# Optimization experiments

Hardware: AMD Instinct MI355X
Metric: run time of the kernel (lower is better)

The kernel has to match this reference:

```python
import jax, jax.numpy as jnp
import numpy as np

B, S = 16384, 6
IN_SIZE = 128
FIN, NFIN, BERT = 84, 11, 768
D = IN_SIZE + FIN + NFIN + BERT  # 991 = mlp_in_dim
NODE_V = 6 * 50000 + 1
FIN_V = 100001
OUT = 2


def setup_inputs() -> dict:
    key = jax.random.key(0)
    ks = jax.random.split(key, 20)
    inp = {}
    inp["node_seq"] = jax.random.randint(ks[0], (B, S), 0, 300000)
    inp["fin_seq"] = jax.random.randint(ks[1], (B, S), 0, 100000)
    inp["nfin_seq"] = jax.random.randint(ks[2], (B, S), 0, 100000)
    inp["mda_seq"] = jax.random.randint(ks[3], (B, S), 0, 100000)
    inp["seq_len"] = 1 + jax.random.randint(ks[4], (B,), 0, S)  # in [1, S]
    # embedding tables
    inp["node_table"] = jax.random.normal(ks[5], (NODE_V, IN_SIZE), jnp.float32) * 0.02
    inp["fin_table"] = jax.random.normal(ks[6], (FIN_V, FIN), jnp.float32) * 0.02
    inp["nfin_table"] = jax.random.normal(ks[7], (FIN_V, NFIN), jnp.float32) * 0.02
    inp["bert_table"] = jax.random.normal(ks[8], (FIN_V, BERT), jnp.float32) * 0.02
    # LayerNorm params
    inp["ln_g"] = jnp.ones((D,), jnp.float32)
    inp["ln_b"] = jnp.zeros((D,), jnp.float32)
    # GRU params (torch layout: [3D, D] for reset|update|new)
    s = 1.0 / np.sqrt(D)
    inp["W_ih"] = jax.random.uniform(ks[9], (3 * D, D), jnp.float32, -s, s)
    inp["W_hh"] = jax.random.uniform(ks[10], (3 * D, D), jnp.float32, -s, s)
    inp["b_ih"] = jax.random.uniform(ks[11], (3 * D,), jnp.float32, -s, s)
    inp["b_hh"] = jax.random.uniform(ks[12], (3 * D,), jnp.float32, -s, s)
    # BatchNorm1d affine params
    inp["bn_g"] = jnp.ones((D,), jnp.float32)
    inp["bn_b"] = jnp.zeros((D,), jnp.float32)
    # MLP: Linear(D, 2D) -> Linear(2D, OUT)
    inp["W1"] = jax.random.uniform(ks[13], (2 * D, D), jnp.float32, -s, s)
    inp["b1"] = jax.random.uniform(ks[14], (2 * D,), jnp.float32, -s, s)
    s2 = 1.0 / np.sqrt(2 * D)
    inp["W2"] = jax.random.uniform(ks[15], (OUT, 2 * D), jnp.float32, -s2, s2)
    inp["b2"] = jax.random.uniform(ks[16], (OUT,), jnp.float32, -s2, s2)
    return inp


def _forward(node_seq, fin_seq, nfin_seq, mda_seq, seq_len,
             node_table, fin_table, nfin_table, bert_table,
             ln_g, ln_b, W_ih, W_hh, b_ih, b_hh, bn_g, bn_b, W1, b1, W2, b2):
    # embedding lookups -> concat  [B, S, D]
    x = jnp.concatenate([
        node_table[node_seq],
        fin_table[fin_seq],
        nfin_table[nfin_seq],
        bert_table[mda_seq],
    ], axis=-1)
    # LayerNorm (eps=1e-5, torch default)
    mu = jnp.mean(x, axis=-1, keepdims=True)
    var = jnp.mean(jnp.square(x - mu), axis=-1, keepdims=True)
    x = (x - mu) * jax.lax.rsqrt(var + 1e-5) * ln_g + ln_b
    # GRU, batch_first; precompute input projections [S, B, 3D]
    xg = jnp.einsum('bsd,gd->sbg', x, W_ih) + b_ih
    h0 = jnp.zeros((x.shape[0], W_hh.shape[1]), x.dtype)
    d = W_hh.shape[1]

    def step(h, xg_t):
        gh = h @ W_hh.T + b_hh
        xr, xz, xn = xg_t[:, :d], xg_t[:, d:2 * d], xg_t[:, 2 * d:]
        hr, hz, hn = gh[:, :d], gh[:, d:2 * d], gh[:, 2 * d:]
        r = jax.nn.sigmoid(xr + hr)
        z = jax.nn.sigmoid(xz + hz)
        n = jnp.tanh(xn + r * hn)
        h = (1.0 - z) * n + z * h
        return h, h

    _, ys = jax.lax.scan(step, h0, xg)          # [S, B, D]
    ys = jnp.transpose(ys, (1, 0, 2))           # [B, S, D]
    # gather_indexes at seq_len - 1
    idx = (seq_len - 1)[:, None, None]
    out = jnp.take_along_axis(ys, idx, axis=1)[:, 0, :]  # [B, D]
    # BatchNorm1d with batch stats (training math), eps=1e-4
    bmu = jnp.mean(out, axis=0)
    bvar = jnp.mean(jnp.square(out - bmu), axis=0)
    out = (out - bmu) * jax.lax.rsqrt(bvar + 1e-4) * bn_g + bn_b
    # MLP: two linears, no activation
    h1 = out @ W1.T + b1
    logits = h1 @ W2.T + b2
    return logits


def reference(node_seq, fin_seq, nfin_seq, mda_seq, seq_len,
              node_table, fin_table, nfin_table, bert_table,
              ln_g, ln_b, W_ih, W_hh, b_ih, b_hh, bn_g, bn_b, W1, b1, W2, b2):
    return _forward(node_seq, fin_seq, nfin_seq, mda_seq, seq_len,
                    node_table, fin_table, nfin_table, bert_table,
                    ln_g, ln_b, W_ih, W_hh, b_ih, b_hh, bn_g, bn_b, W1, b1, W2, b2)
```

## Files before the change

kernel.cpp:

```cpp
#include <hip/hip_runtime.h>
#include <hip/hip_bf16.h>
#include <cstdint>
#include <cstddef>

#define D_   991
#define DP   992
#define GP   3072
#define B_   16384
#define S_   6

typedef __bf16 bf16;
typedef __attribute__((ext_vector_type(8))) __bf16 bf16x8;
typedef __attribute__((ext_vector_type(4))) float f32x4;

#define GLDS16(gp, lp) __builtin_amdgcn_global_load_lds(               \
    (const __attribute__((address_space(1))) void*)(gp),               \
    (__attribute__((address_space(3))) void*)(lp), 16, 0, 0)

__global__ __launch_bounds__(256, 2) void gemm_bt2(
    const bf16* __restrict__ A0, const bf16* __restrict__ W0,
    float* __restrict__ C0,
    const bf16* __restrict__ A1, const bf16* __restrict__ W1,
    float* __restrict__ C1)
{
  __shared__ __align__(16) bf16 As[128 * 32];
  __shared__ __align__(16) bf16 Bs[128 * 32];

  const bf16* A = blockIdx.z ? A1 : A0;
  const bf16* W = blockIdx.z ? W1 : W0;
  float*      C = blockIdx.z ? C1 : C0;

  const int tid  = threadIdx.x;
  const int lane = tid & 63;
  const int wave = tid >> 6;
  const int bm = blockIdx.y;
  const int bn = blockIdx.x;

  const int srow = tid >> 2;
  const int scol = (tid & 3) << 3;
  const bf16* aP = A + (size_t)(bm * 128 + srow) * DP + scol;
  const bf16* bP = W + (size_t)(bn * 128 + srow) * DP + scol;
  bf16* asW = &As[wave * 512];
  bf16* bsW = &Bs[wave * 512];

  const int wr = (wave >> 1) << 6;
  const int wc = (wave & 1) << 6;
  const int frow = lane & 15;
  const int fq   = lane >> 4;

  f32x4 acc[4][4];
#pragma unroll
  for (int i = 0; i < 4; i++)
#pragma unroll
    for (int j = 0; j < 4; j++) acc[i][j] = (f32x4){0.f, 0.f, 0.f, 0.f};

  for (int k0 = 0; k0 < DP; k0 += 32) {
    __syncthreads();
    GLDS16(aP + k0,                     asW);
    GLDS16(aP + (size_t)64 * DP + k0,   asW + 2048);
    GLDS16(bP + k0,                     bsW);
    GLDS16(bP + (size_t)64 * DP + k0,   bsW + 2048);
    __syncthreads();

    bf16x8 af[4], bfr[4];
#pragma unroll
    for (int mt = 0; mt < 4; mt++)
      af[mt] = *(const bf16x8*)&As[(wr + mt * 16 + frow) * 32 + fq * 8];
#pragma unroll
    for (int nt = 0; nt < 4; nt++)
      bfr[nt] = *(const bf16x8*)&Bs[(wc + nt * 16 + frow) * 32 + fq * 8];
#pragma unroll
    for (int mt = 0; mt < 4; mt++)
#pragma unroll
      for (int nt = 0; nt < 4; nt++)
        acc[mt][nt] = __builtin_amdgcn_mfma_f32_16x16x32_bf16(
            af[mt], bfr[nt], acc[mt][nt], 0, 0, 0);
  }

  const int rbase = bm * 128 + wr + fq * 4;
  const int cbase = bn * 128 + wc + frow;
#pragma unroll
  for (int mt = 0; mt < 4; mt++)
#pragma unroll
    for (int nt = 0; nt < 4; nt++) {
      float* cp = C + (size_t)(rbase + mt * 16) * GP + cbase + nt * 16;
#pragma unroll
      for (int i = 0; i < 4; i++) cp[(size_t)i * GP] = acc[mt][nt][i];
    }
}

__global__ __launch_bounds__(256) void pad_w(
    const float* __restrict__ Wih, const float* __restrict__ Whh,
    bf16* __restrict__ Wihp, bf16* __restrict__ Whhp)
{
  int idx = blockIdx.x * 256 + threadIdx.x;
  if (idx >= GP * DP) return;
  int c = idx % DP;
  int p = idx / DP;
  int sec = p >> 10;
  int j = p & 1023;
  bf16 vi = (bf16)0.0f, vh = (bf16)0.0f;
  if (j < D_ && c < D_) {
    size_t src = ((size_t)sec * D_ + j) * D_ + c;
    vi = (bf16)Wih[src];
    vh = (bf16)Whh[src];
  }
  Wihp[idx] = vi;
  Whhp[idx] = vh;
}

#define WCJ 16
__global__ __launch_bounds__(256) void wc_fold(
    const float* __restrict__ W1, const float* __restrict__ b1,
    const float* __restrict__ W2, const float* __restrict__ b2,
    float* __restrict__ wc)
{
  const int o   = blockIdx.y;
  const int j0  = blockIdx.x * WCJ;
  const int tid = threadIdx.x;
  const int jend = min(j0 + WCJ, 2 * D_);

  float acc[4] = {0.f, 0.f, 0.f, 0.f};
  for (int j = j0; j < jend; j++) {
    float w2 = W2[o * 2 * D_ + j];
#pragma unroll
    for (int k = 0; k < 4; k++) {
      int d = tid + (k << 8);
      if (d < D_) acc[k] += w2 * W1[(size_t)j * D_ + d];
    }
  }
#pragma unroll
  for (int k = 0; k < 4; k++) {
    int d = tid + (k << 8);
    if (d < D_) atomicAdd(&wc[o * D_ + d], acc[k]);
  }
  float pb = 0.f;
  if (tid < WCJ && (j0 + tid) < 2 * D_)
    pb = W2[o * 2 * D_ + j0 + tid] * b1[j0 + tid];
  for (int off = 8; off > 0; off >>= 1) pb += __shfl_down(pb, off);
  if (tid == 0) {
    float add = pb + (blockIdx.x == 0 ? b2[o] : 0.f);
    atomicAdd(&wc[2 * D_ + o], add);
  }
}

__global__ __launch_bounds__(256) void embed_ln(
    const int* __restrict__ node_seq, const int* __restrict__ fin_seq,
    const int* __restrict__ nfin_seq, const int* __restrict__ mda_seq,
    const float* __restrict__ node_t, const float* __restrict__ fin_t,
    const float* __restrict__ nfin_t, const float* __restrict__ bert_t,
    const float* __restrict__ ln_g, const float* __restrict__ ln_b,
    bf16* __restrict__ xout, int base, int t)
{
  const int bl = blockIdx.x;
  const int bid = (base + bl) * S_ + t;
  const int tid = threadIdx.x;
  const int ni = node_seq[bid];
  const int fi = fin_seq[bid];
  const int nf = nfin_seq[bid];
  const int mi = mda_seq[bid];

  float v[4];
  float s1 = 0.f, s2 = 0.f;
#pragma unroll
  for (int k = 0; k < 4; k++) {
    int d = tid + (k << 8);
    float val = 0.f;
    if (d < D_) {
      if (d < 128)       val = node_t[(size_t)ni * 128 + d];
      else if (d < 212)  val = fin_t[(size_t)fi * 84 + (d - 128)];
      else if (d < 223)  val = nfin_t[(size_t)nf * 11 + (d - 212)];
      else               val = bert_t[(size_t)mi * 768 + (d - 223)];
    }
    v[k] = val;
    s1 += val;
    s2 += val * val;
  }
#pragma unroll
  for (int off = 32; off > 0; off >>= 1) {
    s1 += __shfl_down(s1, off);
    s2 += __shfl_down(s2, off);
  }
  __shared__ float red[8];
  const int wave = tid >> 6, lane = tid & 63;
  if (lane == 0) { red[wave] = s1; red[4 + wave] = s2; }
  __syncthreads();
  s1 = red[0] + red[1] + red[2] + red[3];
  s2 = red[4] + red[5] + red[6] + red[7];
  const float mean = s1 * (1.0f / D_);
  const float rstd = rsqrtf(s2 * (1.0f / D_) - mean * mean + 1e-5f);

  bf16* row = xout + (size_t)bl * DP;
#pragma unroll
  for (int k = 0; k < 4; k++) {
    int d = tid + (k << 8);
    if (d < D_)
      row[d] = (bf16)(((v[k] - mean) * rstd) * ln_g[d] + ln_b[d]);
    else if (d == D_)
      row[d] = (bf16)0.0f;
  }
}

__global__ __launch_bounds__(256) void gru_gate(
    const float* __restrict__ Gx, const float* __restrict__ Gh,
    const float* __restrict__ b_ih, const float* __restrict__ b_hh,
    float* __restrict__ h, bf16* __restrict__ hb, float* __restrict__ outb,
    const int* __restrict__ seq_len, int base, int t, int first)
{
  const int bl = blockIdx.x;
  const int bg = base + bl;
  const int tid = threadIdx.x;
  const int sel = (seq_len[bg] - 1 == t);
  const float* gx = Gx + (size_t)bl * GP;
  const float* gh = Gh + (size_t)bl * GP;
  const size_t hrow = (size_t)bl * DP;
  const size_t orow = (size_t)bg * DP;

#pragma unroll
  for (int k = 0; k < 4; k++) {
    int d = tid + (k << 8);
    if (d < D_) {
      float xr = gx[d]        + b_ih[d];
      float xz = gx[1024 + d] + b_ih[D_ + d];
      float xn = gx[2048 + d] + b_ih[2 * D_ + d];
      float hr = b_hh[d];
      float hz = b_hh[D_ + d];
      float hn = b_hh[2 * D_ + d];
      float hp = 0.f;
      if (!first) {
        hr += gh[d];
        hz += gh[1024 + d];
        hn += gh[2048 + d];
        hp = h[hrow + d];
      }
      float r = 1.f / (1.f + expf(-(xr + hr)));
      float z = 1.f / (1.f + expf(-(xz + hz)));
      float n = tanhf(xn + r * hn);
      float hv = (1.f - z) * n + z * hp;
      h[hrow + d] = hv;
      hb[hrow + d] = (bf16)hv;
      if (sel) outb[orow + d] = hv;
    } else if (d == D_) {
      h[hrow + d] = 0.f;
      hb[hrow + d] = (bf16)0.0f;
      if (sel) outb[orow + d] = 0.f;
    }
  }
}

__global__ __launch_bounds__(256) void bn_stats(
    const float* __restrict__ outb, float* __restrict__ sums,
    float* __restrict__ sumsq)
{
  const int tid = threadIdx.x;
  const int b0 = blockIdx.x << 6;
  float a[4] = {0.f, 0.f, 0.f, 0.f}, q[4] = {0.f, 0.f, 0.f, 0.f};
  for (int r = 0; r < 64; r++) {
    const float* row = outb + (size_t)(b0 + r) * DP;
#pragma unroll
    for (int k = 0; k < 4; k++) {
      int d = tid + (k << 8);
      if (d < D_) {
        float v = row[d];
        a[k] += v;
        q[k] += v * v;
      }
    }
  }
#pragma unroll
  for (int k = 0; k < 4; k++) {
    int d = tid + (k << 8);
    if (d < D_) {
      atomicAdd(&sums[d], a[k]);
      atomicAdd(&sumsq[d], q[k]);
    }
  }
}

__global__ __launch_bounds__(256) void final_k(
    const float* __restrict__ outb, const float* __restrict__ sums,
    const float* __restrict__ sumsq, const float* __restrict__ bn_g,
    const float* __restrict__ bn_b, const float* __restrict__ wc,
    float* __restrict__ out)
{
  const int wave = threadIdx.x >> 6, lane = threadIdx.x & 63;
  const int b = (blockIdx.x << 2) + wave;
  const float* row = outb + (size_t)b * DP;
  float p0 = 0.f, p1 = 0.f;
  for (int d = lane; d < D_; d += 64) {
    float mean = sums[d] * (1.0f / B_);
    float var  = sumsq[d] * (1.0f / B_) - mean * mean;
    float sc = bn_g[d] * rsqrtf(var + 1e-4f);
    float v = (row[d] - mean) * sc + bn_b[d];
    p0 += v * wc[d];
    p1 += v * wc[D_ + d];
  }
#pragma unroll
  for (int off = 32; off > 0; off >>= 1) {
    p0 += __shfl_down(p0, off);
    p1 += __shfl_down(p1, off);
  }
  if (lane == 0) {
    out[(size_t)b * 2]     = p0 + wc[2 * D_];
    out[(size_t)b * 2 + 1] = p1 + wc[2 * D_ + 1];
  }
}

static inline size_t ws_required(size_t bc) {
  return 77217792ull + bc * 32512ull;
}

extern "C" void kernel_launch(void* const* d_in, const int* in_sizes, int n_in,
                              void* d_out, int out_size, void* d_ws, size_t ws_size,
                              hipStream_t stream)
{
  int bc;
  if      (ws_size >= ws_required(16384)) bc = 16384;
  else if (ws_size >= ws_required(8192))  bc = 8192;
  else if (ws_size >= ws_required(4096))  bc = 4096;
  else {
    hipMemsetAsync(d_out, 0, (size_t)out_size * 2, stream);
    return;
  }
  const int nch = B_ / bc;

  const int*   node_seq = (const int*)d_in[0];
  const int*   fin_seq  = (const int*)d_in[1];
  const int*   nfin_seq = (const int*)d_in[2];
  const int*   mda_seq  = (const int*)d_in[3];
  const int*   seq_len  = (const int*)d_in[4];
  const float* node_t   = (const float*)d_in[5];
  const float* fin_t    = (const float*)d_in[6];
  const float* nfin_t   = (const float*)d_in[7];
  const float* bert_t   = (const float*)d_in[8];
  const float* ln_g     = (const float*)d_in[9];
  const float* ln_b     = (const float*)d_in[10];
  const float* W_ih     = (const float*)d_in[11];
  const float* W_hh     = (const float*)d_in[12];
  const float* b_ih     = (const float*)d_in[13];
  const float* b_hh     = (const float*)d_in[14];
  const float* bn_gv    = (const float*)d_in[15];
  const float* bn_bv    = (const float*)d_in[16];
  const float* W1       = (const float*)d_in[17];
  const float* b1       = (const float*)d_in[18];
  const float* W2       = (const float*)d_in[19];
  const float* b2       = (const float*)d_in[20];

  char* ws = (char*)d_ws;
  size_t off = 0;
  bf16*  Wihp  = (bf16*)(ws + off);  off += (size_t)GP * DP * 2;
  bf16*  Whhp  = (bf16*)(ws + off);  off += (size_t)GP * DP * 2;
  bf16*  xcur  = (bf16*)(ws + off);  off += (size_t)bc * DP * 2;
  float* Gx    = (float*)(ws + off); off += (size_t)bc * GP * 4;
  float* Gh    = (float*)(ws + off); off += (size_t)bc * GP * 4;
  float* h     = (float*)(ws + off); off += (size_t)bc * DP * 4;
  bf16*  hb    = (bf16*)(ws + off);  off += (size_t)bc * DP * 2;
  float* outb  = (float*)(ws + off); off += (size_t)B_ * DP * 4;
  float* bnsum = (float*)(ws + off); off += 8192;
  float* wcbuf = (float*)(ws + off); off += 8192;

  pad_w<<<(GP * DP + 255) / 256, 256, 0, stream>>>(W_ih, W_hh, Wihp, Whhp);
  hipMemsetAsync(bnsum, 0, 16384, stream);
  dim3 wcg((2 * D_ + WCJ - 1) / WCJ, 2);
  wc_fold<<<wcg, 256, 0, stream>>>(W1, b1, W2, b2, wcbuf);

  for (int ch = 0; ch < nch; ch++) {
    const int base = ch * bc;
    for (int t = 0; t < S_; t++) {
      embed_ln<<<bc, 256, 0, stream>>>(node_seq, fin_seq, nfin_seq, mda_seq,
                                       node_t, fin_t, nfin_t, bert_t,
                                       ln_g, ln_b, xcur, base, t);
      dim3 g2(GP / 128, bc / 128, t > 0 ? 2 : 1);
      gemm_bt2<<<g2, 256, 0, stream>>>(xcur, Wihp, Gx, hb, Whhp, Gh);
      gru_gate<<<bc, 256, 0, stream>>>(Gx, Gh, b_ih, b_hh, h, hb, outb,
                                       seq_len, base, t, t == 0 ? 1 : 0);
    }
  }

  bn_stats<<<256, 256, 0, stream>>>(outb, bnsum, bnsum + 1024);
  final_k<<<B_ / 4, 256, 0, stream>>>(outb, bnsum, bnsum + 1024,
                                      bn_gv, bn_bv, wcbuf, (float*)d_out);
}
```

Baseline: 3.031 ms.

## Fuse input and hidden GRU GEMMs into one concatenated-K GEMM

Concatenates x and h into one activation buffer of width 2048 and builds a combined weight matrix. The r and z gate rows use K=2048, so the x and h contributions are summed inside the GEMM, and the n gate keeps separate x and h outputs. This removes the separate Gh buffer, halves the output writes and reads for r/z, and replaces two GEMM passes with one. In exchange, each k-loop iteration pads 991 up to 1024 per half, and the Wcat layout adds 4096 weight rows.

```diff
diff --git a/kernel.cpp b/kernel.cpp
--- a/kernel.cpp
+++ b/kernel.cpp
@@ -4,10 +4,11 @@
 #include <cstddef>
 
 #define D_   991
-#define DP   992
-#define GP   3072
 #define B_   16384
 #define S_   6
+#define KP   2048
+#define GPN  4096
+#define WROWS 4096
 
 typedef __bf16 bf16;
 typedef __attribute__((ext_vector_type(8))) __bf16 bf16x8;
@@ -17,29 +18,28 @@
     (const __attribute__((address_space(1))) void*)(gp),               \
     (__attribute__((address_space(3))) void*)(lp), 16, 0, 0)
 
-__global__ __launch_bounds__(256, 2) void gemm_bt2(
-    const bf16* __restrict__ A0, const bf16* __restrict__ W0,
-    float* __restrict__ C0,
-    const bf16* __restrict__ A1, const bf16* __restrict__ W1,
-    float* __restrict__ C1)
+__global__ __launch_bounds__(256, 2) void gemm_cat(
+    const bf16* __restrict__ A, const bf16* __restrict__ W,
+    float* __restrict__ C, int first)
 {
   __shared__ __align__(16) bf16 As[128 * 32];
   __shared__ __align__(16) bf16 Bs[128 * 32];
-
-  const bf16* A = blockIdx.z ? A1 : A0;
-  const bf16* W = blockIdx.z ? W1 : W0;
-  float*      C = blockIdx.z ? C1 : C0;
 
   const int tid  = threadIdx.x;
   const int lane = tid & 63;
   const int wave = tid >> 6;
+  const int bn = blockIdx.x;
   const int bm = blockIdx.y;
-  const int bn = blockIdx.x;
+
+  int ks, ke;
+  if (bn < 16)      { ks = 0;    ke = first ? 1024 : 2048; }
+  else if (bn < 24) { ks = 0;    ke = 1024; }
+  else              { ks = 1024; ke = 2048; }
 
   const int srow = tid >> 2;
   const int scol = (tid & 3) << 3;
-  const bf16* aP = A + (size_t)(bm * 128 + srow) * DP + scol;
-  const bf16* bP = W + (size_t)(bn * 128 + srow) * DP + scol;
+  const bf16* aP = A + (size_t)(bm * 128 + srow) * KP + scol;
+  const bf16* bP = W + (size_t)(bn * 128 + srow) * KP + scol;
   bf16* asW = &As[wave * 512];
   bf16* bsW = &Bs[wave * 512];
 
@@ -54,12 +54,12 @@
 #pragma unroll
     for (int j = 0; j < 4; j++) acc[i][j] = (f32x4){0.f, 0.f, 0.f, 0.f};
 
-  for (int k0 = 0; k0 < DP; k0 += 32) {
+  for (int k0 = ks; k0 < ke; k0 += 32) {
     __syncthreads();
-    GLDS16(aP + k0,                     asW);
-    GLDS16(aP + (size_t)64 * DP + k0,   asW + 2048);
-    GLDS16(bP + k0,                     bsW);
-    GLDS16(bP + (size_t)64 * DP + k0,   bsW + 2048);
+    GLDS16(aP + k0,                    asW);
+    GLDS16(aP + (size_t)64 * KP + k0,  asW + 2048);
+    GLDS16(bP + k0,                    bsW);
+    GLDS16(bP + (size_t)64 * KP + k0,  bsW + 2048);
     __syncthreads();
 
     bf16x8 af[4], bfr[4];
@@ -83,30 +83,32 @@
   for (int mt = 0; mt < 4; mt++)
 #pragma unroll
     for (int nt = 0; nt < 4; nt++) {
-      float* cp = C + (size_t)(rbase + mt * 16) * GP + cbase + nt * 16;
-#pragma unroll
-      for (int i = 0; i < 4; i++) cp[(size_t)i * GP] = acc[mt][nt][i];
-    }
-}
-
-__global__ __launch_bounds__(256) void pad_w(
+      float* cp = C + (size_t)(rbase + mt * 16) * GPN + cbase + nt * 16;
+#pragma unroll
+      for (int i = 0; i < 4; i++) cp[(size_t)i * GPN] = acc[mt][nt][i];
+    }
+}
+
+__global__ __launch_bounds__(256) void pad_wcat(
     const float* __restrict__ Wih, const float* __restrict__ Whh,
-    bf16* __restrict__ Wihp, bf16* __restrict__ Whhp)
+    bf16* __restrict__ Wc)
 {
   int idx = blockIdx.x * 256 + threadIdx.x;
-  if (idx >= GP * DP) return;
-  int c = idx % DP;
-  int p = idx / DP;
-  int sec = p >> 10;
-  int j = p & 1023;
-  bf16 vi = (bf16)0.0f, vh = (bf16)0.0f;
-  if (j < D_ && c < D_) {
-    size_t src = ((size_t)sec * D_ + j) * D_ + c;
-    vi = (bf16)Wih[src];
-    vh = (bf16)Whh[src];
-  }
-  Wihp[idx] = vi;
-  Whhp[idx] = vh;
+  int c = idx & (KP - 1);
+  int r = idx >> 11;
+  int sec = r >> 10;
+  int j = r & 1023;
+  float v = 0.f;
+  if (j < D_) {
+    if (c < D_) {
+      int g = (sec == 0) ? 0 : (sec == 1) ? 1 : (sec == 2) ? 2 : -1;
+      if (g >= 0) v = Wih[((size_t)g * D_ + j) * D_ + c];
+    } else if (c >= 1024 && c < 1024 + D_) {
+      int g = (sec == 0) ? 0 : (sec == 1) ? 1 : (sec == 3) ? 2 : -1;
+      if (g >= 0) v = Whh[((size_t)g * D_ + j) * D_ + (c - 1024)];
+    }
+  }
+  Wc[idx] = (bf16)v;
 }
 
 #define WCJ 16
@@ -150,7 +152,7 @@
     const float* __restrict__ node_t, const float* __restrict__ fin_t,
     const float* __restrict__ nfin_t, const float* __restrict__ bert_t,
     const float* __restrict__ ln_g, const float* __restrict__ ln_b,
-    bf16* __restrict__ xout, int base, int t)
+    bf16* __restrict__ acat, int base, int t)
 {
   const int bl = blockIdx.x;
   const int bid = (base + bl) * S_ + t;
@@ -190,60 +192,51 @@
   const float mean = s1 * (1.0f / D_);
   const float rstd = rsqrtf(s2 * (1.0f / D_) - mean * mean + 1e-5f);
 
-  bf16* row = xout + (size_t)bl * DP;
+  bf16* row = acat + (size_t)bl * KP;
 #pragma unroll
   for (int k = 0; k < 4; k++) {
     int d = tid + (k << 8);
     if (d < D_)
       row[d] = (bf16)(((v[k] - mean) * rstd) * ln_g[d] + ln_b[d]);
-    else if (d == D_)
+    else
       row[d] = (bf16)0.0f;
   }
 }
 
 __global__ __launch_bounds__(256) void gru_gate(
-    const float* __restrict__ Gx, const float* __restrict__ Gh,
-    const float* __restrict__ b_ih, const float* __restrict__ b_hh,
-    float* __restrict__ h, bf16* __restrict__ hb, float* __restrict__ outb,
+    const float* __restrict__ G, const float* __restrict__ b_ih,
+    const float* __restrict__ b_hh, float* __restrict__ h,
+    bf16* __restrict__ acat, float* __restrict__ outb,
     const int* __restrict__ seq_len, int base, int t, int first)
 {
   const int bl = blockIdx.x;
   const int bg = base + bl;
   const int tid = threadIdx.x;
   const int sel = (seq_len[bg] - 1 == t);
-  const float* gx = Gx + (size_t)bl * GP;
-  const float* gh = Gh + (size_t)bl * GP;
-  const size_t hrow = (size_t)bl * DP;
-  const size_t orow = (size_t)bg * DP;
+  const float* g = G + (size_t)bl * GPN;
+  float* hrow = h + (size_t)bl * 1024;
+  bf16*  hbr  = acat + (size_t)bl * KP + 1024;
+  float* orow = outb + (size_t)bg * 1024;
 
 #pragma unroll
   for (int k = 0; k < 4; k++) {
     int d = tid + (k << 8);
     if (d < D_) {
-      float xr = gx[d]        + b_ih[d];
-      float xz = gx[1024 + d] + b_ih[D_ + d];
-      float xn = gx[2048 + d] + b_ih[2 * D_ + d];
-      float hr = b_hh[d];
-      float hz = b_hh[D_ + d];
-      float hn = b_hh[2 * D_ + d];
-      float hp = 0.f;
-      if (!first) {
-        hr += gh[d];
-        hz += gh[1024 + d];
-        hn += gh[2048 + d];
-        hp = h[hrow + d];
-      }
-      float r = 1.f / (1.f + expf(-(xr + hr)));
-      float z = 1.f / (1.f + expf(-(xz + hz)));
-      float n = tanhf(xn + r * hn);
+      float rpre = g[d]        + b_ih[d]          + b_hh[d];
+      float zpre = g[1024 + d] + b_ih[D_ + d]     + b_hh[D_ + d];
+      float nx   = g[2048 + d] + b_ih[2 * D_ + d];
+      float nh   = (first ? 0.f : g[3072 + d]) + b_hh[2 * D_ + d];
+      float hp   = first ? 0.f : hrow[d];
+      float r = 1.f / (1.f + expf(-rpre));
+      float z = 1.f / (1.f + expf(-zpre));
+      float n = tanhf(nx + r * nh);
       float hv = (1.f - z) * n + z * hp;
-      h[hrow + d] = hv;
-      hb[hrow + d] = (bf16)hv;
-      if (sel) outb[orow + d] = hv;
-    } else if (d == D_) {
-      h[hrow + d] = 0.f;
-      hb[hrow + d] = (bf16)0.0f;
-      if (sel) outb[orow + d] = 0.f;
+      hrow[d] = hv;
+      hbr[d]  = (bf16)hv;
+      if (sel) orow[d] = hv;
+    } else {
+      hbr[d] = (bf16)0.0f;
+      if (sel) orow[d] = 0.f;
     }
   }
 }
@@ -256,7 +249,7 @@
   const int b0 = blockIdx.x << 6;
   float a[4] = {0.f, 0.f, 0.f, 0.f}, q[4] = {0.f, 0.f, 0.f, 0.f};
   for (int r = 0; r < 64; r++) {
-    const float* row = outb + (size_t)(b0 + r) * DP;
+    const float* row = outb + (size_t)(b0 + r) * 1024;
 #pragma unroll
     for (int k = 0; k < 4; k++) {
       int d = tid + (k << 8);
@@ -285,7 +278,7 @@
 {
   const int wave = threadIdx.x >> 6, lane = threadIdx.x & 63;
   const int b = (blockIdx.x << 2) + wave;
-  const float* row = outb + (size_t)b * DP;
+  const float* row = outb + (size_t)b * 1024;
   float p0 = 0.f, p1 = 0.f;
   for (int d = lane; d < D_; d += 64) {
     float mean = sums[d] * (1.0f / B_);
@@ -307,7 +300,7 @@
 }
 
 static inline size_t ws_required(size_t bc) {
-  return 77217792ull + bc * 32512ull;
+  return 83902464ull + bc * 24576ull;
 }
 
 extern "C" void kernel_launch(void* const* d_in, const int* in_sizes, int n_in,
@@ -348,18 +341,15 @@
 
   char* ws = (char*)d_ws;
   size_t off = 0;
-  bf16*  Wihp  = (bf16*)(ws + off);  off += (size_t)GP * DP * 2;
-  bf16*  Whhp  = (bf16*)(ws + off);  off += (size_t)GP * DP * 2;
-  bf16*  xcur  = (bf16*)(ws + off);  off += (size_t)bc * DP * 2;
-  float* Gx    = (float*)(ws + off); off += (size_t)bc * GP * 4;
-  float* Gh    = (float*)(ws + off); off += (size_t)bc * GP * 4;
-  float* h     = (float*)(ws + off); off += (size_t)bc * DP * 4;
-  bf16*  hb    = (bf16*)(ws + off);  off += (size_t)bc * DP * 2;
-  float* outb  = (float*)(ws + off); off += (size_t)B_ * DP * 4;
+  bf16*  Wcat  = (bf16*)(ws + off);  off += (size_t)WROWS * KP * 2;
+  bf16*  Acat  = (bf16*)(ws + off);  off += (size_t)bc * KP * 2;
+  float* G     = (float*)(ws + off); off += (size_t)bc * GPN * 4;
+  float* h     = (float*)(ws + off); off += (size_t)bc * 1024 * 4;
+  float* outb  = (float*)(ws + off); off += (size_t)B_ * 1024 * 4;
   float* bnsum = (float*)(ws + off); off += 8192;
   float* wcbuf = (float*)(ws + off); off += 8192;
 
-  pad_w<<<(GP * DP + 255) / 256, 256, 0, stream>>>(W_ih, W_hh, Wihp, Whhp);
+  pad_wcat<<<(WROWS * KP) / 256, 256, 0, stream>>>(W_ih, W_hh, Wcat);
   hipMemsetAsync(bnsum, 0, 16384, stream);
   dim3 wcg((2 * D_ + WCJ - 1) / WCJ, 2);
   wc_fold<<<wcg, 256, 0, stream>>>(W1, b1, W2, b2, wcbuf);
@@ -367,13 +357,14 @@
   for (int ch = 0; ch < nch; ch++) {
     const int base = ch * bc;
     for (int t = 0; t < S_; t++) {
+      const int first = (t == 0) ? 1 : 0;
       embed_ln<<<bc, 256, 0, stream>>>(node_seq, fin_seq, nfin_seq, mda_seq,
                                        node_t, fin_t, nfin_t, bert_t,
-                                       ln_g, ln_b, xcur, base, t);
-      dim3 g2(GP / 128, bc / 128, t > 0 ? 2 : 1);
-      gemm_bt2<<<g2, 256, 0, stream>>>(xcur, Wihp, Gx, hb, Whhp, Gh);
-      gru_gate<<<bc, 256, 0, stream>>>(Gx, Gh, b_ih, b_hh, h, hb, outb,
-                                       seq_len, base, t, t == 0 ? 1 : 0);
+                                       ln_g, ln_b, Acat, base, t);
+      dim3 gg(first ? 24 : 32, bc / 128);
+      gemm_cat<<<gg, 256, 0, stream>>>(Acat, Wcat, G, first);
+      gru_gate<<<bc, 256, 0, stream>>>(G, b_ih, b_hh, h, Acat, outb,
+                                       seq_len, base, t, first);
     }
   }
 
```

Result: faster. 2.911 ms (-4.0%).
